# Performance work log

Hardware: AMD Instinct MI355X
Metric: run time of the kernel (lower is better)

## Reference

```python
import jax, jax.numpy as jnp
import numpy as np

K = 3   # bil_filt_size
NL = 1  # n_layers (bil_filt_size == 2*n_layers + 1 required for shape consistency)


def _conv3d_relu(x, w, b):
    # Conv3d(1,1,kernel=3,stride=1,valid) + ReLU, NCDHW layout
    y = jax.lax.conv_general_dilated(
        x, w, window_strides=(1, 1, 1), padding='VALID',
        dimension_numbers=('NCDHW', 'OIDHW', 'NCDHW'))
    return jax.nn.relu(y + b[None, :, None, None, None])


def setup_inputs() -> dict:
    key = jax.random.key(0)
    ks = jax.random.split(key, 7)
    B, D, H, W = 2, 18, 128, 128
    Dout = D - 2 * NL            # 16
    M = B * Dout * H * W         # 524288 per-voxel neighborhoods
    s = K + 2 * NL               # 5: conv shrinks s -> K
    x = jax.random.normal(ks[0], (B, 1, D, H, W), dtype=jnp.float32)
    domain_neighbor = jax.random.uniform(ks[1], (M, 1, s, s, s), dtype=jnp.float32)
    guide_im = jax.random.normal(ks[2], (M, 1, s, s, s), dtype=jnp.float32)
    dom_w = jax.random.normal(ks[3], (1, 1, 3, 3, 3), dtype=jnp.float32) * 0.1
    dom_b = jnp.full((1,), 0.01, dtype=jnp.float32)
    rng_w = jax.random.normal(ks[4], (1, 1, 3, 3, 3), dtype=jnp.float32) * 0.1
    rng_b = jnp.full((1,), 0.01, dtype=jnp.float32)
    return {'x': x, 'domain_neighbor': domain_neighbor, 'guide_im': guide_im,
            'dom_w': dom_w, 'dom_b': dom_b, 'rng_w': rng_w, 'rng_b': rng_b}


def reference(x, domain_neighbor, guide_im, dom_w, dom_b, rng_w, rng_b):
    B, _, D, H, W = x.shape
    Dout = D - 2 * NL
    # learned bilateral weights per voxel: [M,1,K,K,K]
    domain_kernel = _conv3d_relu(domain_neighbor, dom_w, dom_b)
    range_kernel = _conv3d_relu(guide_im, rng_w, rng_b)
    weights = domain_kernel * range_kernel + 1e-10
    # unfold order in torch is (B, C=1, Dout, H, W, k, k, k) -> reshape(-1,1,k,k,k)
    Wr = weights.reshape(B, Dout, H, W, K, K, K)
    pad = K // 2
    # pad H and W only (no depth padding), matching F.pad(..., (p,p,p,p,0,0))
    xp = jnp.pad(x[:, 0], ((0, 0), (0, 0), (pad, pad), (pad, pad)))  # [B,D,H+2p,W+2p]
    # fused weighted local sum: avoid materializing the K^3-unfolded tensor
    num = jnp.zeros((B, Dout, H, W), dtype=x.dtype)
    for i in range(K):
        for j in range(K):
            for l in range(K):
                num = num + Wr[..., i, j, l] * xp[:, i:i + Dout, j:j + H, l:l + W]
    den = Wr.sum(axis=(-3, -2, -1))
    return (num / den)[:, None]  # [B,1,Dout,H,W]
```

## Files before the change

### kernel.cpp

```cpp
#include <hip/hip_runtime.h>


#define VPB 64
#define REC 125
#define CHUNK_F4 2000

__global__ __launch_bounds__(64) void jbf_kernel(
    const float* __restrict__ x,
    const float* __restrict__ dom,
    const float* __restrict__ gui,
    const float* __restrict__ dom_w,
    const float* __restrict__ dom_b,
    const float* __restrict__ rng_w,
    const float* __restrict__ rng_b,
    float* __restrict__ out)
{
    __shared__ float sm[VPB * REC];
    const int lane = threadIdx.x;
    const int m0   = blockIdx.x * VPB;
    const int m    = m0 + lane;

    float wd[27], wr[27];
#pragma unroll
    for (int i = 0; i < 27; ++i) { wd[i] = dom_w[i]; wr[i] = rng_w[i]; }
    const float bd = dom_b[0], br = rng_b[0];

    {
        const float4* src = (const float4*)(dom + (size_t)m0 * REC);
        float4* dst = (float4*)sm;
#pragma unroll
        for (int k = 0; k < 31; ++k) dst[k * 64 + lane] = src[k * 64 + lane];
        if (lane < CHUNK_F4 - 31 * 64) dst[31 * 64 + lane] = src[31 * 64 + lane];
    }
    __syncthreads();

    float dkv[27];
#pragma unroll
    for (int i = 0; i < 27; ++i) dkv[i] = 0.f;
    {
        const float* rec = sm + lane * REC;
#pragma unroll
        for (int z = 0; z < 5; ++z)
#pragma unroll
            for (int r = 0; r < 5; ++r)
#pragma unroll
                for (int c = 0; c < 5; ++c) {
                    const float v = rec[z * 25 + r * 5 + c];
#pragma unroll
                    for (int i = 0; i < 3; ++i) {
                        const int a = z - i; if (a < 0 || a > 2) continue;
#pragma unroll
                        for (int j = 0; j < 3; ++j) {
                            const int b = r - j; if (b < 0 || b > 2) continue;
#pragma unroll
                            for (int l = 0; l < 3; ++l) {
                                const int cc = c - l; if (cc < 0 || cc > 2) continue;
                                dkv[(i * 3 + j) * 3 + l] =
                                    fmaf(v, wd[(a * 3 + b) * 3 + cc],
                                         dkv[(i * 3 + j) * 3 + l]);
                            }
                        }
                    }
                }
    }
    __syncthreads();

    {
        const float4* src = (const float4*)(gui + (size_t)m0 * REC);
        float4* dst = (float4*)sm;
#pragma unroll
        for (int k = 0; k < 31; ++k) dst[k * 64 + lane] = src[k * 64 + lane];
        if (lane < CHUNK_F4 - 31 * 64) dst[31 * 64 + lane] = src[31 * 64 + lane];
    }
    __syncthreads();

    float rkv[27];
#pragma unroll
    for (int i = 0; i < 27; ++i) rkv[i] = 0.f;
    {
        const float* rec = sm + lane * REC;
#pragma unroll
        for (int z = 0; z < 5; ++z)
#pragma unroll
            for (int r = 0; r < 5; ++r)
#pragma unroll
                for (int c = 0; c < 5; ++c) {
                    const float v = rec[z * 25 + r * 5 + c];
#pragma unroll
                    for (int i = 0; i < 3; ++i) {
                        const int a = z - i; if (a < 0 || a > 2) continue;
#pragma unroll
                        for (int j = 0; j < 3; ++j) {
                            const int b = r - j; if (b < 0 || b > 2) continue;
#pragma unroll
                            for (int l = 0; l < 3; ++l) {
                                const int cc = c - l; if (cc < 0 || cc > 2) continue;
                                rkv[(i * 3 + j) * 3 + l] =
                                    fmaf(v, wr[(a * 3 + b) * 3 + cc],
                                         rkv[(i * 3 + j) * 3 + l]);
                            }
                        }
                    }
                }
    }

    const int w_  = m & 127;
    const int h_  = (m >> 7) & 127;
    const int dz  = (m >> 14) & 15;
    const int b_  = m >> 18;

    float num = 0.f, den = 0.f;
#pragma unroll
    for (int i = 0; i < 3; ++i) {
        const int zz = b_ * 18 + dz + i;
#pragma unroll
        for (int j = 0; j < 3; ++j) {
            const int hh = h_ - 1 + j;
            const bool okh = (unsigned)hh < 128u;
#pragma unroll
            for (int l = 0; l < 3; ++l) {
                const int ww = w_ - 1 + l;
                const bool ok = okh && ((unsigned)ww < 128u);
                const float xv = ok ? x[((size_t)zz * 128 + hh) * 128 + ww] : 0.f;
                const float wv = fmaxf(dkv[(i * 3 + j) * 3 + l] + bd, 0.f) *
                                 fmaxf(rkv[(i * 3 + j) * 3 + l] + br, 0.f) + 1e-10f;
                den += wv;
                num = fmaf(wv, xv, num);
            }
        }
    }
    out[m] = num / den;
}

extern "C" void kernel_launch(void* const* d_in, const int* in_sizes, int n_in,
                              void* d_out, int out_size, void* d_ws, size_t ws_size,
                              hipStream_t stream) {
    const float* x     = (const float*)d_in[0];
    const float* dom   = (const float*)d_in[1];
    const float* gui   = (const float*)d_in[2];
    const float* dom_w = (const float*)d_in[3];
    const float* dom_b = (const float*)d_in[4];
    const float* rng_w = (const float*)d_in[5];
    const float* rng_b = (const float*)d_in[6];
    float* outp = (float*)d_out;

    const int M = in_sizes[1] / REC;
    const int grid = M / VPB;
    jbf_kernel<<<grid, VPB, 0, stream>>>(x, dom, gui, dom_w, dom_b,
                                         rng_w, rng_b, outp);
}
```

Before: 513.7 us.

## Stage records in 32-float chunks via direct global-to-LDS loads with XOR swizzle

Replaces the single 32KB LDS staging of 64 full 125-float records with four passes of 32-float slices. Each slice is loaded through global_load_lds directly into a small 8KB buffer, using an XOR swizzle to avoid bank conflicts. The 125th element is loaded separately per thread, and the two convolutions share one loop. The smaller LDS footprint and launch_bounds(64,4) aim to raise occupancy and hide latency, at the cost of many more barriers and narrower 4-byte global loads.

Result: slower. 952.6 us (+85.4%).

```diff
diff --git a/kernel.cpp b/kernel.cpp
--- a/kernel.cpp
+++ b/kernel.cpp
@@ -3,9 +3,58 @@
 
 #define VPB 64
 #define REC 125
-#define CHUNK_F4 2000
 
-__global__ __launch_bounds__(64) void jbf_kernel(
+#define GAS(p) ((const __attribute__((address_space(1))) float*)(p))
+#define LAS(p) ((__attribute__((address_space(3))) float*)(p))
+
+template <int F0>
+__device__ __forceinline__ void stage32(const float* __restrict__ src, int m0,
+                                        float* lds, int lane)
+{
+    const int half = lane >> 5;
+    const int sl   = lane & 31;
+#pragma unroll
+    for (int k = 0; k < 32; ++k) {
+        const int v = 2 * k + half;
+        int fo = sl ^ ((2 * k) & 31) ^ half;
+        if (F0 == 96) fo = fo < 27 ? fo : 27;
+        const float* g = src + (size_t)(m0 + v) * REC + F0 + fo;
+        __builtin_amdgcn_global_load_lds(GAS(g), LAS(lds + k * 64), 4, 0, 0);
+    }
+}
+
+template <int F0>
+__device__ __forceinline__ void conv_part(const float* __restrict__ sbuf, int lane,
+                                          const float* __restrict__ w, float* acc)
+{
+    const int xs   = lane & 31;
+    const int base = lane * 32;
+#pragma unroll
+    for (int c0 = 0; c0 < 32; ++c0) {
+        const int f = F0 + c0;
+        if (f >= 124) continue;
+        const float v = sbuf[base + (c0 ^ xs)];
+        const int z  = f / 25;
+        const int r  = (f % 25) / 5;
+        const int c5 = f % 5;
+#pragma unroll
+        for (int i = 0; i < 3; ++i) {
+            const int a = z - i; if (a < 0 || a > 2) continue;
+#pragma unroll
+            for (int j = 0; j < 3; ++j) {
+                const int b = r - j; if (b < 0 || b > 2) continue;
+#pragma unroll
+                for (int l = 0; l < 3; ++l) {
+                    const int cc = c5 - l; if (cc < 0 || cc > 2) continue;
+                    acc[(i * 3 + j) * 3 + l] =
+                        fmaf(v, w[(a * 3 + b) * 3 + cc], acc[(i * 3 + j) * 3 + l]);
+                }
+            }
+        }
+    }
+}
+
+__global__ __launch_bounds__(64, 4) void jbf_kernel(
     const float* __restrict__ x,
     const float* __restrict__ dom,
     const float* __restrict__ gui,
@@ -15,99 +64,60 @@
     const float* __restrict__ rng_b,
     float* __restrict__ out)
 {
-    __shared__ float sm[VPB * REC];
+    __shared__ float sm[VPB * 32];
     const int lane = threadIdx.x;
     const int m0   = blockIdx.x * VPB;
     const int m    = m0 + lane;
 
-    float wd[27], wr[27];
-#pragma unroll
-    for (int i = 0; i < 27; ++i) { wd[i] = dom_w[i]; wr[i] = rng_w[i]; }
     const float bd = dom_b[0], br = rng_b[0];
 
-    {
-        const float4* src = (const float4*)(dom + (size_t)m0 * REC);
-        float4* dst = (float4*)sm;
+    const float d124 = dom[(size_t)m * REC + 124];
+    const float g124 = gui[(size_t)m * REC + 124];
+
+    float dkv[27], acc[27];
+
+#pragma unroll 1
+    for (int p = 0; p < 2; ++p) {
+        const float* __restrict__ src  = p ? gui : dom;
+        const float* __restrict__ wsrc = p ? rng_w : dom_w;
+        float w[27];
 #pragma unroll
-        for (int k = 0; k < 31; ++k) dst[k * 64 + lane] = src[k * 64 + lane];
-        if (lane < CHUNK_F4 - 31 * 64) dst[31 * 64 + lane] = src[31 * 64 + lane];
-    }
-    __syncthreads();
+        for (int i = 0; i < 27; ++i) w[i] = wsrc[i];
+#pragma unroll
+        for (int i = 0; i < 27; ++i) acc[i] = 0.f;
 
-    float dkv[27];
+        stage32<0>(src, m0, sm, lane);
+        __syncthreads();
+        conv_part<0>(sm, lane, w, acc);
+        __syncthreads();
+
+        stage32<32>(src, m0, sm, lane);
+        __syncthreads();
+        conv_part<32>(sm, lane, w, acc);
+        __syncthreads();
+
+        stage32<64>(src, m0, sm, lane);
+        __syncthreads();
+        conv_part<64>(sm, lane, w, acc);
+        __syncthreads();
+
+        stage32<96>(src, m0, sm, lane);
+        __syncthreads();
+        conv_part<96>(sm, lane, w, acc);
+        __syncthreads();
+
+        acc[26] = fmaf(p ? g124 : d124, w[26], acc[26]);
+
+        if (p == 0) {
 #pragma unroll
-    for (int i = 0; i < 27; ++i) dkv[i] = 0.f;
-    {
-        const float* rec = sm + lane * REC;
-#pragma unroll
-        for (int z = 0; z < 5; ++z)
-#pragma unroll
-            for (int r = 0; r < 5; ++r)
-#pragma unroll
-                for (int c = 0; c < 5; ++c) {
-                    const float v = rec[z * 25 + r * 5 + c];
-#pragma unroll
-                    for (int i = 0; i < 3; ++i) {
-                        const int a = z - i; if (a < 0 || a > 2) continue;
-#pragma unroll
-                        for (int j = 0; j < 3; ++j) {
-                            const int b = r - j; if (b < 0 || b > 2) continue;
-#pragma unroll
-                            for (int l = 0; l < 3; ++l) {
-                                const int cc = c - l; if (cc < 0 || cc > 2) continue;
-                                dkv[(i * 3 + j) * 3 + l] =
-                                    fmaf(v, wd[(a * 3 + b) * 3 + cc],
-                                         dkv[(i * 3 + j) * 3 + l]);
-                            }
-                        }
-                    }
-                }
-    }
-    __syncthreads();
-
-    {
-        const float4* src = (const float4*)(gui + (size_t)m0 * REC);
-        float4* dst = (float4*)sm;
-#pragma unroll
-        for (int k = 0; k < 31; ++k) dst[k * 64 + lane] = src[k * 64 + lane];
-        if (lane < CHUNK_F4 - 31 * 64) dst[31 * 64 + lane] = src[31 * 64 + lane];
-    }
-    __syncthreads();
-
-    float rkv[27];
-#pragma unroll
-    for (int i = 0; i < 27; ++i) rkv[i] = 0.f;
-    {
-        const float* rec = sm + lane * REC;
-#pragma unroll
-        for (int z = 0; z < 5; ++z)
-#pragma unroll
-            for (int r = 0; r < 5; ++r)
-#pragma unroll
-                for (int c = 0; c < 5; ++c) {
-                    const float v = rec[z * 25 + r * 5 + c];
-#pragma unroll
-                    for (int i = 0; i < 3; ++i) {
-                        const int a = z - i; if (a < 0 || a > 2) continue;
-#pragma unroll
-                        for (int j = 0; j < 3; ++j) {
-                            const int b = r - j; if (b < 0 || b > 2) continue;
-#pragma unroll
-                            for (int l = 0; l < 3; ++l) {
-                                const int cc = c - l; if (cc < 0 || cc > 2) continue;
-                                rkv[(i * 3 + j) * 3 + l] =
-                                    fmaf(v, wr[(a * 3 + b) * 3 + cc],
-                                         rkv[(i * 3 + j) * 3 + l]);
-                            }
-                        }
-                    }
-                }
+            for (int i = 0; i < 27; ++i) dkv[i] = acc[i];
+        }
     }
 
-    const int w_  = m & 127;
-    const int h_  = (m >> 7) & 127;
-    const int dz  = (m >> 14) & 15;
-    const int b_  = m >> 18;
+    const int w_ = m & 127;
+    const int h_ = (m >> 7) & 127;
+    const int dz = (m >> 14) & 15;
+    const int b_ = m >> 18;
 
     float num = 0.f, den = 0.f;
 #pragma unroll
@@ -123,7 +133,7 @@
                 const bool ok = okh && ((unsigned)ww < 128u);
                 const float xv = ok ? x[((size_t)zz * 128 + hh) * 128 + ww] : 0.f;
                 const float wv = fmaxf(dkv[(i * 3 + j) * 3 + l] + bd, 0.f) *
-                                 fmaxf(rkv[(i * 3 + j) * 3 + l] + br, 0.f) + 1e-10f;
+                                 fmaxf(acc[(i * 3 + j) * 3 + l] + br, 0.f) + 1e-10f;
                 den += wv;
                 num = fmaf(wv, xv, num);
             }
```
